# Kernel tuning notes

Hardware: AMD Instinct MI355X
Metric: run time of the kernel (lower is better)

The kernel has to match this reference:

```python
import jax, jax.numpy as jnp
import numpy as np

T, B, D_IN, D_LAT = 512, 64, 512, 1024


def setup_inputs() -> dict:
    key = jax.random.key(0)
    ks = jax.random.split(key, 9)
    s_in = 1.0 / np.sqrt(D_IN + D_LAT)
    inp = {
        "x": jax.random.normal(ks[0], (T, B, D_IN), dtype=jnp.float32),
        "Wf": jax.random.normal(ks[1], (D_LAT, D_IN + D_LAT), dtype=jnp.float32) * s_in,
        "bf": jax.random.normal(ks[2], (D_LAT,), dtype=jnp.float32) * s_in,
        "Wi": jax.random.normal(ks[3], (D_LAT, D_IN + D_LAT), dtype=jnp.float32) * s_in,
        "bi": jax.random.normal(ks[4], (D_LAT,), dtype=jnp.float32) * s_in,
        "Wc": jax.random.normal(ks[5], (D_LAT, D_IN + D_LAT), dtype=jnp.float32) * s_in,
        "bc": jax.random.normal(ks[6], (D_LAT,), dtype=jnp.float32) * s_in,
        "Wo": jax.random.normal(ks[7], (D_LAT, D_IN + D_LAT), dtype=jnp.float32) * s_in,
        "bo": jax.random.normal(ks[8], (D_LAT,), dtype=jnp.float32) * s_in,
    }
    return inp


def reference(x, Wf, bf, Wi, bi, Wc, bc, Wo, bo):
    # x: [T, B, D_in]. Same math as 4 separate gate linears on concat(x, h),
    # expressed as one fused gate GEMM per step (concat weights along out dim).
    length, batch, _ = x.shape
    latent = Wf.shape[0]
    W = jnp.concatenate([Wf, Wi, Wc, Wo], axis=0)            # [4L, D_in+L]
    b = jnp.concatenate([bf, bi, bc, bo], axis=0)            # [4L]
    Wx, Wh = W[:, : x.shape[-1]], W[:, x.shape[-1]:]         # split concat input
    # Precompute input contribution for all timesteps: [T, B, 4L]
    xg = jnp.einsum('tbd,gd->tbg', x, Wx) + b

    def step(carry, xg_t):
        h, c = carry
        g = xg_t + h @ Wh.T                                   # [B, 4L]
        f = jax.nn.sigmoid(g[:, 0 * latent:1 * latent])
        i = jax.nn.sigmoid(g[:, 1 * latent:2 * latent])
        cand = jnp.tanh(g[:, 2 * latent:3 * latent])
        o = jax.nn.sigmoid(g[:, 3 * latent:4 * latent])
        c_new = f * c + i * cand
        h_new = o * jnp.tanh(c_new)
        return (h_new, c_new), h_new

    h0 = jnp.zeros((batch, latent), dtype=x.dtype)
    c0 = jnp.zeros((batch, latent), dtype=x.dtype)  # self.ct zeros init
    _, hs = jax.lax.scan(step, (h0, c0), xg)
    return hs  # [T, B, latent]
```

## Files before the change

kernel.cpp:

```cpp
#include <hip/hip_runtime.h>
#include <hip/hip_bf16.h>


typedef __attribute__((ext_vector_type(8))) short short8;
typedef __attribute__((ext_vector_type(4))) short short4v;
typedef __attribute__((ext_vector_type(4))) float f32x4;

#define T_STEPS 512
#define BATCH   64
#define DIN     512
#define DLAT    1024
#define NWG     128
#define LPW     8

#define WS_H    4096
#define WS_XG   (4096 + 262144)

#define MFMA(a, b, c) __builtin_amdgcn_mfma_f32_16x16x32_bf16((a), (b), (c), 0, 0, 0)

static __device__ __forceinline__ unsigned short f2bf(float f) {
  unsigned u = __builtin_bit_cast(unsigned, f);
  u = (u + 0x7FFFu + ((u >> 16) & 1u)) >> 16;
  return (unsigned short)u;
}
static __device__ __forceinline__ float bf2f(unsigned short s) {
  unsigned u = ((unsigned)s) << 16;
  return __builtin_bit_cast(float, u);
}
static __device__ __forceinline__ float sigf(float x) {
  return 1.0f / (1.0f + __expf(-x));
}
static __device__ __forceinline__ float tanhfast(float x) {
  return 2.0f / (1.0f + __expf(-2.0f * x)) - 1.0f;
}
static __device__ __forceinline__ short8 packbf(f32x4 a, f32x4 b) {
  short8 s;
  s[0]=(short)f2bf(a[0]); s[1]=(short)f2bf(a[1]); s[2]=(short)f2bf(a[2]); s[3]=(short)f2bf(a[3]);
  s[4]=(short)f2bf(b[0]); s[5]=(short)f2bf(b[1]); s[6]=(short)f2bf(b[2]); s[7]=(short)f2bf(b[3]);
  return s;
}

__global__ __launch_bounds__(256, 2) void lstm_phase1(
    const float* __restrict__ x,
    const float* __restrict__ Wf, const float* __restrict__ bfp,
    const float* __restrict__ Wi, const float* __restrict__ bip,
    const float* __restrict__ Wc, const float* __restrict__ bcp,
    const float* __restrict__ Wo, const float* __restrict__ bop,
    unsigned short* __restrict__ xg)
{
  __shared__ __align__(16) short lds[BATCH * DIN];
  const int tid  = threadIdx.x;
  const int nb   = blockIdx.x;
  const int tb4  = blockIdx.y;
  const int lane = tid & 63;
  const int wv   = tid >> 6;
  const int cc   = lane & 15;
  const int q    = lane >> 4;

  const int wg = nb * 4 + wv;
  const int jj = wg * LPW + (cc & 7);
  short8 bw[2][16];
  #pragma unroll
  for (int T = 0; T < 2; ++T) {
    const float* Wp = (T == 0) ? (cc < 8 ? Wf : Wi) : (cc < 8 ? Wc : Wo);
    const float* base = Wp + (size_t)jj * (DIN + DLAT);
    #pragma unroll
    for (int k = 0; k < 16; ++k) {
      const f32x4* p = (const f32x4*)(base + k * 32 + q * 8);
      bw[T][k] = packbf(p[0], p[1]);
    }
  }
  float biasv[2];
  biasv[0] = (cc < 8 ? bfp : bip)[jj];
  biasv[1] = (cc < 8 ? bcp : bop)[jj];

  for (int tt = 0; tt < 4; ++tt) {
    const int tb = tb4 * 4 + tt;

    const float* xs = x + (size_t)tb * (BATCH * DIN);
    #pragma unroll
    for (int it = 0; it < 16; ++it) {
      int c = tid + 256 * it;
      int row = c >> 6, kc = c & 63;
      const f32x4* p = (const f32x4*)(xs + row * DIN + kc * 8);
      f32x4 v0 = p[0], v1 = p[1];
      int byte = (row * (DIN * 2) + kc * 16) ^ ((row & 7) << 4);
      *(short8*)((char*)lds + byte) = packbf(v0, v1);
    }
    __syncthreads();

    f32x4 acc[4][2] = {};
    #pragma unroll
    for (int k = 0; k < 16; ++k) {
      #pragma unroll
      for (int m = 0; m < 4; ++m) {
        int row = m * 16 + cc;
        int byte = (row * (DIN * 2) + (k * 32 + q * 8) * 2) ^ ((row & 7) << 4);
        short8 a = *(const short8*)((const char*)lds + byte);
        acc[m][0] = MFMA(a, bw[0][k], acc[m][0]);
        acc[m][1] = MFMA(a, bw[1][k], acc[m][1]);
      }
    }
    __syncthreads();

    #pragma unroll
    for (int T = 0; T < 2; ++T) {
      float bias = biasv[T];
      #pragma unroll
      for (int m = 0; m < 4; ++m) {
        f32x4 g = acc[m][T];
        short4v s;
        s[0] = (short)f2bf(g[0] + bias);
        s[1] = (short)f2bf(g[1] + bias);
        s[2] = (short)f2bf(g[2] + bias);
        s[3] = (short)f2bf(g[3] + bias);
        size_t idx = ((((size_t)tb * NWG + wg) * 4 + m) * 2 + T) * 64 + lane;
        *(short4v*)(xg + idx * 4) = s;
      }
    }
  }
}

__global__ __launch_bounds__(256, 1) void lstm_phase2(
    const float* __restrict__ Wf, const float* __restrict__ Wi,
    const float* __restrict__ Wc, const float* __restrict__ Wo,
    const unsigned short* __restrict__ xg,
    unsigned short* __restrict__ hbuf,
    unsigned int* __restrict__ flags,
    float* __restrict__ out)
{
  const int tid  = threadIdx.x;
  const int lane = tid & 63;
  const int wv   = tid >> 6;
  const int wg   = blockIdx.x;
  const int cc   = lane & 15;
  const int q    = lane >> 4;
  const int jj   = wg * LPW + (cc & 7);

  __shared__ unsigned short lds_h[4][16][8];
  __shared__ float          lds_o[4][16][8];

  short8 wh[2][32];
  #pragma unroll
  for (int T = 0; T < 2; ++T) {
    const float* Wp = (T == 0) ? (cc < 8 ? Wf : Wi) : (cc < 8 ? Wc : Wo);
    const float* base = Wp + (size_t)jj * (DIN + DLAT) + DIN;
    #pragma unroll
    for (int k = 0; k < 32; ++k) {
      const f32x4* p = (const f32x4*)(base + k * 32 + q * 8);
      wh[T][k] = packbf(p[0], p[1]);
    }
  }

  f32x4 cst = {0.f, 0.f, 0.f, 0.f};
  const unsigned short* xbase = xg + (((size_t)wg * 4 + wv) * 2) * 256 + (size_t)lane * 4;
  const int arow = wv * 16 + cc;

  short4v xp0 = *(const short4v*)(xbase);
  short4v xp1 = *(const short4v*)(xbase + 256);

  for (int t = 0; t < T_STEPS; ++t) {
    if (t > 0) {
      if (wv == 0) {
        const unsigned int* fp = flags + lane;
        for (;;) {
          unsigned a1 = __hip_atomic_load(fp,      __ATOMIC_RELAXED, __HIP_MEMORY_SCOPE_AGENT);
          unsigned a2 = __hip_atomic_load(fp + 64, __ATOMIC_RELAXED, __HIP_MEMORY_SCOPE_AGENT);
          if (__all(a1 >= (unsigned)t && a2 >= (unsigned)t)) break;
          __builtin_amdgcn_s_sleep(1);
        }
      }
      __syncthreads();
    }

    f32x4 acc0 = {0.f,0.f,0.f,0.f}, acc1 = {0.f,0.f,0.f,0.f};
    if (t > 0) {
      const unsigned long long* hq = (const unsigned long long*)
          (hbuf + (((t & 1) ^ 1) << 16) + arow * DLAT);
      short8 a[16];
      #pragma unroll
      for (int k = 0; k < 16; ++k) {
        unsigned long long lo = __hip_atomic_load(hq + q*2 + k*8,     __ATOMIC_RELAXED, __HIP_MEMORY_SCOPE_AGENT);
        unsigned long long hi = __hip_atomic_load(hq + q*2 + k*8 + 1, __ATOMIC_RELAXED, __HIP_MEMORY_SCOPE_AGENT);
        union { unsigned long long u[2]; short8 s; } cv; cv.u[0]=lo; cv.u[1]=hi;
        a[k] = cv.s;
      }
      #pragma unroll
      for (int k = 0; k < 16; ++k) {
        acc0 = MFMA(a[k], wh[0][k], acc0);
        acc1 = MFMA(a[k], wh[1][k], acc1);
      }
      #pragma unroll
      for (int k = 0; k < 16; ++k) {
        unsigned long long lo = __hip_atomic_load(hq + q*2 + (16+k)*8,     __ATOMIC_RELAXED, __HIP_MEMORY_SCOPE_AGENT);
        unsigned long long hi = __hip_atomic_load(hq + q*2 + (16+k)*8 + 1, __ATOMIC_RELAXED, __HIP_MEMORY_SCOPE_AGENT);
        union { unsigned long long u[2]; short8 s; } cv; cv.u[0]=lo; cv.u[1]=hi;
        a[k] = cv.s;
      }
      #pragma unroll
      for (int k = 0; k < 16; ++k) {
        acc0 = MFMA(a[k], wh[0][16 + k], acc0);
        acc1 = MFMA(a[k], wh[1][16 + k], acc1);
      }
    }

    f32x4 g0, g1;
    #pragma unroll
    for (int r = 0; r < 4; ++r) {
      g0[r] = acc0[r] + bf2f((unsigned short)xp0[r]);
      g1[r] = acc1[r] + bf2f((unsigned short)xp1[r]);
    }

    f32x4 g0x, g1x;
    #pragma unroll
    for (int r = 0; r < 4; ++r) {
      g0x[r] = __shfl_xor(g0[r], 8, 64);
      g1x[r] = __shfl_xor(g1[r], 8, 64);
    }
    const bool lo = (cc < 8);
    float hv[4];
    #pragma unroll
    for (int r = 0; r < 4; ++r) {
      float fpre = lo ? g0[r]  : g0x[r];
      float ipre = lo ? g0x[r] : g0[r];
      float cpre = lo ? g1[r]  : g1x[r];
      float opre = lo ? g1x[r] : g1[r];
      float fg = sigf(fpre), ig = sigf(ipre), cd = tanhfast(cpre), og = sigf(opre);
      float cn = fg * cst[r] + ig * cd;
      cst[r] = cn;
      hv[r] = og * tanhfast(cn);
    }

    if (lo) {
      #pragma unroll
      for (int r = 0; r < 4; ++r) {
        lds_h[wv][q * 4 + r][cc] = f2bf(hv[r]);
        lds_o[wv][q * 4 + r][cc] = hv[r];
      }
    }
    __syncthreads();

    {
      unsigned short* hw = hbuf + ((t & 1) << 16);
      float* op = out + (size_t)t * (BATCH * DLAT);
      if (lane < 32) {
        int row = lane >> 1, half = lane & 1;
        unsigned long long v = *(const unsigned long long*)&lds_h[wv][row][half * 4];
        int b = wv * 16 + row;
        __hip_atomic_store((unsigned long long*)(hw + b * DLAT + wg * LPW + half * 4), v,
                           __ATOMIC_RELAXED, __HIP_MEMORY_SCOPE_AGENT);
      }
      {
        int row = lane >> 2, quarter = lane & 3;
        unsigned long long v = *(const unsigned long long*)&lds_o[wv][row][quarter * 2];
        int b = wv * 16 + row;
        *(unsigned long long*)(op + b * DLAT + wg * LPW + quarter * 2) = v;
      }
    }

    asm volatile("s_waitcnt vmcnt(0)" ::: "memory");
    __syncthreads();
    if (tid == 0)
      __hip_atomic_store(flags + wg, (unsigned)(t + 1), __ATOMIC_RELAXED, __HIP_MEMORY_SCOPE_AGENT);

    {
      int tn = (t + 1 < T_STEPS) ? t + 1 : t;
      const unsigned short* xn = xbase + ((size_t)tn << 18);
      xp0 = *(const short4v*)(xn);
      xp1 = *(const short4v*)(xn + 256);
    }
  }
}

extern "C" void kernel_launch(void* const* d_in, const int* in_sizes, int n_in,
                              void* d_out, int out_size, void* d_ws, size_t ws_size,
                              hipStream_t stream) {
  (void)in_sizes; (void)n_in; (void)out_size; (void)ws_size;
  const float* x   = (const float*)d_in[0];
  const float* Wf  = (const float*)d_in[1];
  const float* bfp = (const float*)d_in[2];
  const float* Wi  = (const float*)d_in[3];
  const float* bip = (const float*)d_in[4];
  const float* Wc  = (const float*)d_in[5];
  const float* bcp = (const float*)d_in[6];
  const float* Wo  = (const float*)d_in[7];
  const float* bop = (const float*)d_in[8];
  float* out = (float*)d_out;

  unsigned int*   flags = (unsigned int*)d_ws;
  unsigned short* hbuf  = (unsigned short*)((char*)d_ws + WS_H);
  unsigned short* xg    = (unsigned short*)((char*)d_ws + WS_XG);

  hipMemsetAsync(d_ws, 0, 4096, stream);
  lstm_phase1<<<dim3(32, 128), 256, 0, stream>>>(x, Wf, bfp, Wi, bip, Wc, bcp, Wo, bop, xg);
  lstm_phase2<<<dim3(NWG), 256, 0, stream>>>(Wf, Wi, Wc, Wo, xg, hbuf, flags, out);
}
```

Before: 6.313 ms.

## Shrink recurrent grid to 32 workgroups with LDS-staged swizzled h broadcast

The recurrent phase now runs on 32 workgroups instead of 128. Each wave owns 8 latent units across all 64 batch rows, giving 4 M-tiles per wave. The full h vector is bulk-copied from global into a swizzled LDS staging buffer in two halves, and MFMA A-operands are read from LDS. Each wave no longer issues its own per-lane global atomic loads. The aim is to cut the grid-barrier fan-in (fewer flags to poll) and redundant global h reads. The cost is 4x more MFMA work per workgroup on the serial critical path, plus extra syncthreads.

```diff
diff --git a/kernel.cpp b/kernel.cpp
--- a/kernel.cpp
+++ b/kernel.cpp
@@ -5,18 +5,20 @@
 typedef __attribute__((ext_vector_type(8))) short short8;
 typedef __attribute__((ext_vector_type(4))) short short4v;
 typedef __attribute__((ext_vector_type(4))) float f32x4;
+typedef unsigned long long ull;
 
 #define T_STEPS 512
 #define BATCH   64
 #define DIN     512
 #define DLAT    1024
-#define NWG     128
-#define LPW     8
+#define NWG2    32
 
 #define WS_H    4096
 #define WS_XG   (4096 + 262144)
 
 #define MFMA(a, b, c) __builtin_amdgcn_mfma_f32_16x16x32_bf16((a), (b), (c), 0, 0, 0)
+#define AT_LD(p)    __hip_atomic_load((p), __ATOMIC_RELAXED, __HIP_MEMORY_SCOPE_AGENT)
+#define AT_ST(p, v) __hip_atomic_store((p), (v), __ATOMIC_RELAXED, __HIP_MEMORY_SCOPE_AGENT)
 
 static __device__ __forceinline__ unsigned short f2bf(float f) {
   unsigned u = __builtin_bit_cast(unsigned, f);
@@ -58,7 +60,7 @@
   const int q    = lane >> 4;
 
   const int wg = nb * 4 + wv;
-  const int jj = wg * LPW + (cc & 7);
+  const int jj = wg * 8 + (cc & 7);
   short8 bw[2][16];
   #pragma unroll
   for (int T = 0; T < 2; ++T) {
@@ -76,7 +78,6 @@
 
   for (int tt = 0; tt < 4; ++tt) {
     const int tb = tb4 * 4 + tt;
-
     const float* xs = x + (size_t)tb * (BATCH * DIN);
     #pragma unroll
     for (int it = 0; it < 16; ++it) {
@@ -114,8 +115,8 @@
         s[1] = (short)f2bf(g[1] + bias);
         s[2] = (short)f2bf(g[2] + bias);
         s[3] = (short)f2bf(g[3] + bias);
-        size_t idx = ((((size_t)tb * NWG + wg) * 4 + m) * 2 + T) * 64 + lane;
-        *(short4v*)(xg + idx * 4) = s;
+        size_t idx = (size_t)tb * 1024 + (size_t)wg * 8 + m * 2 + T;
+        *(short4v*)(xg + idx * 256 + lane * 4) = s;
       }
     }
   }
@@ -129,16 +130,18 @@
     unsigned int* __restrict__ flags,
     float* __restrict__ out)
 {
+  __shared__ __align__(16) ull stage[8192];
+  unsigned short* lds_h = (unsigned short*)stage;
+  float*          lds_o = (float*)((char*)stage + 4096);
+
   const int tid  = threadIdx.x;
   const int lane = tid & 63;
   const int wv   = tid >> 6;
   const int wg   = blockIdx.x;
   const int cc   = lane & 15;
   const int q    = lane >> 4;
-  const int jj   = wg * LPW + (cc & 7);
-
-  __shared__ unsigned short lds_h[4][16][8];
-  __shared__ float          lds_o[4][16][8];
+  const int swz  = (cc & 7) << 4;
+  const int jj   = wg * 32 + wv * 8 + (cc & 7);
 
   short8 wh[2][32];
   #pragma unroll
@@ -152,123 +155,138 @@
     }
   }
 
-  f32x4 cst = {0.f, 0.f, 0.f, 0.f};
-  const unsigned short* xbase = xg + (((size_t)wg * 4 + wv) * 2) * 256 + (size_t)lane * 4;
-  const int arow = wv * 16 + cc;
-
-  short4v xp0 = *(const short4v*)(xbase);
-  short4v xp1 = *(const short4v*)(xbase + 256);
+  f32x4 cst[4] = {};
+  const unsigned short* xbase = xg + (size_t)(wg * 32 + wv * 8) * 256 + lane * 4;
+  short4v xp0[4], xp1[4];
+  #pragma unroll
+  for (int m = 0; m < 4; ++m) {
+    xp0[m] = *(const short4v*)(xbase + (m * 2 + 0) * 256);
+    xp1[m] = *(const short4v*)(xbase + (m * 2 + 1) * 256);
+  }
+
+  const ull* hb = (const ull*)hbuf;
 
   for (int t = 0; t < T_STEPS; ++t) {
+    f32x4 acc[4][2] = {};
+
     if (t > 0) {
-      if (wv == 0) {
-        const unsigned int* fp = flags + lane;
+      {
+        const unsigned int* fp = flags + (lane & 31);
         for (;;) {
-          unsigned a1 = __hip_atomic_load(fp,      __ATOMIC_RELAXED, __HIP_MEMORY_SCOPE_AGENT);
-          unsigned a2 = __hip_atomic_load(fp + 64, __ATOMIC_RELAXED, __HIP_MEMORY_SCOPE_AGENT);
-          if (__all(a1 >= (unsigned)t && a2 >= (unsigned)t)) break;
+          unsigned a = AT_LD(fp);
+          if (__all(a >= (unsigned)t)) break;
           __builtin_amdgcn_s_sleep(1);
         }
       }
+      const ull* hsrc = hb + (size_t)((t & 1) ^ 1) * 16384;
+      const char* sb = (const char*)stage;
+      ull areg[32];
+
+      #pragma unroll
+      for (int i = 0; i < 32; ++i) areg[i] = AT_LD(hsrc + i * 256 + tid);
+      #pragma unroll
+      for (int i = 0; i < 32; ++i) stage[i * 256 + tid] = areg[i];
       __syncthreads();
-    }
-
-    f32x4 acc0 = {0.f,0.f,0.f,0.f}, acc1 = {0.f,0.f,0.f,0.f};
-    if (t > 0) {
-      const unsigned long long* hq = (const unsigned long long*)
-          (hbuf + (((t & 1) ^ 1) << 16) + arow * DLAT);
-      short8 a[16];
-      #pragma unroll
-      for (int k = 0; k < 16; ++k) {
-        unsigned long long lo = __hip_atomic_load(hq + q*2 + k*8,     __ATOMIC_RELAXED, __HIP_MEMORY_SCOPE_AGENT);
-        unsigned long long hi = __hip_atomic_load(hq + q*2 + k*8 + 1, __ATOMIC_RELAXED, __HIP_MEMORY_SCOPE_AGENT);
-        union { unsigned long long u[2]; short8 s; } cv; cv.u[0]=lo; cv.u[1]=hi;
-        a[k] = cv.s;
-      }
-      #pragma unroll
-      for (int k = 0; k < 16; ++k) {
-        acc0 = MFMA(a[k], wh[0][k], acc0);
-        acc1 = MFMA(a[k], wh[1][k], acc1);
-      }
-      #pragma unroll
-      for (int k = 0; k < 16; ++k) {
-        unsigned long long lo = __hip_atomic_load(hq + q*2 + (16+k)*8,     __ATOMIC_RELAXED, __HIP_MEMORY_SCOPE_AGENT);
-        unsigned long long hi = __hip_atomic_load(hq + q*2 + (16+k)*8 + 1, __ATOMIC_RELAXED, __HIP_MEMORY_SCOPE_AGENT);
-        union { unsigned long long u[2]; short8 s; } cv; cv.u[0]=lo; cv.u[1]=hi;
-        a[k] = cv.s;
-      }
-      #pragma unroll
-      for (int k = 0; k < 16; ++k) {
-        acc0 = MFMA(a[k], wh[0][16 + k], acc0);
-        acc1 = MFMA(a[k], wh[1][16 + k], acc1);
-      }
-    }
-
-    f32x4 g0, g1;
-    #pragma unroll
-    for (int r = 0; r < 4; ++r) {
-      g0[r] = acc0[r] + bf2f((unsigned short)xp0[r]);
-      g1[r] = acc1[r] + bf2f((unsigned short)xp1[r]);
-    }
-
-    f32x4 g0x, g1x;
-    #pragma unroll
-    for (int r = 0; r < 4; ++r) {
-      g0x[r] = __shfl_xor(g0[r], 8, 64);
-      g1x[r] = __shfl_xor(g1[r], 8, 64);
-    }
+
+      #pragma unroll
+      for (int i = 0; i < 32; ++i) areg[i] = AT_LD(hsrc + 8192 + i * 256 + tid);
+      #pragma unroll
+      for (int m = 0; m < 2; ++m) {
+        const int rb = (m * 16 + cc) * 2048;
+        #pragma unroll
+        for (int k = 0; k < 32; ++k) {
+          short8 a = *(const short8*)(sb + ((rb + k * 64 + q * 16) ^ swz));
+          acc[m][0] = MFMA(a, wh[0][k], acc[m][0]);
+          acc[m][1] = MFMA(a, wh[1][k], acc[m][1]);
+        }
+      }
+      __syncthreads();
+
+      #pragma unroll
+      for (int i = 0; i < 32; ++i) stage[i * 256 + tid] = areg[i];
+      __syncthreads();
+      #pragma unroll
+      for (int m = 2; m < 4; ++m) {
+        const int rb = ((m - 2) * 16 + cc) * 2048;
+        #pragma unroll
+        for (int k = 0; k < 32; ++k) {
+          short8 a = *(const short8*)(sb + ((rb + k * 64 + q * 16) ^ swz));
+          acc[m][0] = MFMA(a, wh[0][k], acc[m][0]);
+          acc[m][1] = MFMA(a, wh[1][k], acc[m][1]);
+        }
+      }
+      __syncthreads();
+    }
+
     const bool lo = (cc < 8);
-    float hv[4];
-    #pragma unroll
-    for (int r = 0; r < 4; ++r) {
-      float fpre = lo ? g0[r]  : g0x[r];
-      float ipre = lo ? g0x[r] : g0[r];
-      float cpre = lo ? g1[r]  : g1x[r];
-      float opre = lo ? g1x[r] : g1[r];
-      float fg = sigf(fpre), ig = sigf(ipre), cd = tanhfast(cpre), og = sigf(opre);
-      float cn = fg * cst[r] + ig * cd;
-      cst[r] = cn;
-      hv[r] = og * tanhfast(cn);
-    }
-
-    if (lo) {
+    #pragma unroll
+    for (int m = 0; m < 4; ++m) {
+      f32x4 g0, g1;
       #pragma unroll
       for (int r = 0; r < 4; ++r) {
-        lds_h[wv][q * 4 + r][cc] = f2bf(hv[r]);
-        lds_o[wv][q * 4 + r][cc] = hv[r];
+        g0[r] = acc[m][0][r] + bf2f((unsigned short)xp0[m][r]);
+        g1[r] = acc[m][1][r] + bf2f((unsigned short)xp1[m][r]);
+      }
+      f32x4 g0x, g1x;
+      #pragma unroll
+      for (int r = 0; r < 4; ++r) {
+        g0x[r] = __shfl_xor(g0[r], 8, 64);
+        g1x[r] = __shfl_xor(g1[r], 8, 64);
+      }
+      float hv[4];
+      #pragma unroll
+      for (int r = 0; r < 4; ++r) {
+        float fpre = lo ? g0[r]  : g0x[r];
+        float ipre = lo ? g0x[r] : g0[r];
+        float cpre = lo ? g1[r]  : g1x[r];
+        float opre = lo ? g1x[r] : g1[r];
+        float fg = sigf(fpre), ig = sigf(ipre), cd = tanhfast(cpre), og = sigf(opre);
+        float cn = fg * cst[m][r] + ig * cd;
+        cst[m][r] = cn;
+        hv[r] = og * tanhfast(cn);
+      }
+      if (lo) {
+        #pragma unroll
+        for (int r = 0; r < 4; ++r) {
+          int b = m * 16 + q * 4 + r;
+          lds_h[b * 32 + wv * 8 + cc] = f2bf(hv[r]);
+          lds_o[b * 32 + wv * 8 + cc] = hv[r];
+        }
       }
     }
     __syncthreads();
 
     {
-      unsigned short* hw = hbuf + ((t & 1) << 16);
-      float* op = out + (size_t)t * (BATCH * DLAT);
-      if (lane < 32) {
-        int row = lane >> 1, half = lane & 1;
-        unsigned long long v = *(const unsigned long long*)&lds_h[wv][row][half * 4];
-        int b = wv * 16 + row;
-        __hip_atomic_store((unsigned long long*)(hw + b * DLAT + wg * LPW + half * 4), v,
-                           __ATOMIC_RELAXED, __HIP_MEMORY_SCOPE_AGENT);
-      }
-      {
-        int row = lane >> 2, quarter = lane & 3;
-        unsigned long long v = *(const unsigned long long*)&lds_o[wv][row][quarter * 2];
-        int b = wv * 16 + row;
-        *(unsigned long long*)(op + b * DLAT + wg * LPW + quarter * 2) = v;
-      }
-    }
-
+      const int row = tid >> 2, i = tid & 3;
+      ull v0 = ((const ull*)lds_h)[row * 8 + i * 2 + 0];
+      ull v1 = ((const ull*)lds_h)[row * 8 + i * 2 + 1];
+      char* hw = (char*)hbuf + (size_t)(t & 1) * 131072;
+      int base = row * 2048 + wg * 64 + i * 16;
+      AT_ST((ull*)(hw + ((base + 0) ^ ((row & 7) << 4))), v0);
+      AT_ST((ull*)(hw + ((base + 8) ^ ((row & 7) << 4))), v1);
+    }
     asm volatile("s_waitcnt vmcnt(0)" ::: "memory");
     __syncthreads();
-    if (tid == 0)
-      __hip_atomic_store(flags + wg, (unsigned)(t + 1), __ATOMIC_RELAXED, __HIP_MEMORY_SCOPE_AGENT);
-
+    if (tid == 0) AT_ST(flags + wg, (unsigned)(t + 1));
+
+    {
+      const int row = tid >> 2, i = tid & 3;
+      const f32x4* src = (const f32x4*)(lds_o + row * 32 + i * 8);
+      f32x4 o0 = src[0], o1 = src[1];
+      float* op = out + (size_t)t * (BATCH * DLAT) + row * DLAT + wg * 32 + i * 8;
+      *(f32x4*)op = o0;
+      *(f32x4*)(op + 4) = o1;
+    }
     {
       int tn = (t + 1 < T_STEPS) ? t + 1 : t;
       const unsigned short* xn = xbase + ((size_t)tn << 18);
-      xp0 = *(const short4v*)(xn);
-      xp1 = *(const short4v*)(xn + 256);
-    }
+      #pragma unroll
+      for (int m = 0; m < 4; ++m) {
+        xp0[m] = *(const short4v*)(xn + (m * 2 + 0) * 256);
+        xp1[m] = *(const short4v*)(xn + (m * 2 + 1) * 256);
+      }
+    }
+    __syncthreads();
   }
 }
 
@@ -293,5 +311,5 @@
 
   hipMemsetAsync(d_ws, 0, 4096, stream);
   lstm_phase1<<<dim3(32, 128), 256, 0, stream>>>(x, Wf, bfp, Wi, bip, Wc, bcp, Wo, bop, xg);
-  lstm_phase2<<<dim3(NWG), 256, 0, stream>>>(Wf, Wi, Wc, Wo, xg, hbuf, flags, out);
-}
+  lstm_phase2<<<dim3(NWG2), 256, 0, stream>>>(Wf, Wi, Wc, Wo, xg, hbuf, flags, out);
+}
```

After: 9.007 ms. 42.7% more time.

## Read recurrent h from fp32 output instead of separate bf16 h buffer

Applied to the files above, without the earlier changes.

Removes the separate double-buffered bf16 hidden-state buffer. Each step now reads h(t-1) directly from the fp32 output tensor and converts it to bf16 in registers with v_cvt_pk_bf16_f32. All four waves poll the flags themselves, which replaces the wave-0 poll followed by a barrier, and the output store becomes an agent-scope atomic store. This cuts one global write stream and one LDS staging array per step, but each step must read twice as many bytes of h, uses plain (non-atomic) loads for cross-block data, and adds a barrier at the end of each step.

```diff
diff --git a/kernel.cpp b/kernel.cpp
--- a/kernel.cpp
+++ b/kernel.cpp
@@ -5,18 +5,19 @@
 typedef __attribute__((ext_vector_type(8))) short short8;
 typedef __attribute__((ext_vector_type(4))) short short4v;
 typedef __attribute__((ext_vector_type(4))) float f32x4;
+typedef unsigned long long ull;
 
 #define T_STEPS 512
 #define BATCH   64
 #define DIN     512
 #define DLAT    1024
 #define NWG     128
-#define LPW     8
-
-#define WS_H    4096
-#define WS_XG   (4096 + 262144)
+
+#define WS_XG   4096
 
 #define MFMA(a, b, c) __builtin_amdgcn_mfma_f32_16x16x32_bf16((a), (b), (c), 0, 0, 0)
+#define AT_LD(p)    __hip_atomic_load((p), __ATOMIC_RELAXED, __HIP_MEMORY_SCOPE_AGENT)
+#define AT_ST(p, v) __hip_atomic_store((p), (v), __ATOMIC_RELAXED, __HIP_MEMORY_SCOPE_AGENT)
 
 static __device__ __forceinline__ unsigned short f2bf(float f) {
   unsigned u = __builtin_bit_cast(unsigned, f);
@@ -38,6 +39,14 @@
   s[0]=(short)f2bf(a[0]); s[1]=(short)f2bf(a[1]); s[2]=(short)f2bf(a[2]); s[3]=(short)f2bf(a[3]);
   s[4]=(short)f2bf(b[0]); s[5]=(short)f2bf(b[1]); s[6]=(short)f2bf(b[2]); s[7]=(short)f2bf(b[3]);
   return s;
+}
+static __device__ __forceinline__ short8 cvt8(f32x4 a, f32x4 b) {
+  union { unsigned u[4]; short8 s; } r;
+  asm("v_cvt_pk_bf16_f32 %0, %1, %2" : "=v"(r.u[0]) : "v"(a[0]), "v"(a[1]));
+  asm("v_cvt_pk_bf16_f32 %0, %1, %2" : "=v"(r.u[1]) : "v"(a[2]), "v"(a[3]));
+  asm("v_cvt_pk_bf16_f32 %0, %1, %2" : "=v"(r.u[2]) : "v"(b[0]), "v"(b[1]));
+  asm("v_cvt_pk_bf16_f32 %0, %1, %2" : "=v"(r.u[3]) : "v"(b[2]), "v"(b[3]));
+  return r.s;
 }
 
 __global__ __launch_bounds__(256, 2) void lstm_phase1(
@@ -58,7 +67,7 @@
   const int q    = lane >> 4;
 
   const int wg = nb * 4 + wv;
-  const int jj = wg * LPW + (cc & 7);
+  const int jj = wg * 8 + (cc & 7);
   short8 bw[2][16];
   #pragma unroll
   for (int T = 0; T < 2; ++T) {
@@ -76,7 +85,6 @@
 
   for (int tt = 0; tt < 4; ++tt) {
     const int tb = tb4 * 4 + tt;
-
     const float* xs = x + (size_t)tb * (BATCH * DIN);
     #pragma unroll
     for (int it = 0; it < 16; ++it) {
@@ -125,20 +133,18 @@
     const float* __restrict__ Wf, const float* __restrict__ Wi,
     const float* __restrict__ Wc, const float* __restrict__ Wo,
     const unsigned short* __restrict__ xg,
-    unsigned short* __restrict__ hbuf,
     unsigned int* __restrict__ flags,
     float* __restrict__ out)
 {
+  __shared__ float lds_o[4][16][8];
+
   const int tid  = threadIdx.x;
   const int lane = tid & 63;
   const int wv   = tid >> 6;
   const int wg   = blockIdx.x;
   const int cc   = lane & 15;
   const int q    = lane >> 4;
-  const int jj   = wg * LPW + (cc & 7);
-
-  __shared__ unsigned short lds_h[4][16][8];
-  __shared__ float          lds_o[4][16][8];
+  const int jj   = wg * 8 + (cc & 7);
 
   short8 wh[2][32];
   #pragma unroll
@@ -160,47 +166,34 @@
   short4v xp1 = *(const short4v*)(xbase + 256);
 
   for (int t = 0; t < T_STEPS; ++t) {
+    f32x4 acc0 = {0.f,0.f,0.f,0.f}, acc1 = {0.f,0.f,0.f,0.f};
+
     if (t > 0) {
-      if (wv == 0) {
+      {
         const unsigned int* fp = flags + lane;
         for (;;) {
-          unsigned a1 = __hip_atomic_load(fp,      __ATOMIC_RELAXED, __HIP_MEMORY_SCOPE_AGENT);
-          unsigned a2 = __hip_atomic_load(fp + 64, __ATOMIC_RELAXED, __HIP_MEMORY_SCOPE_AGENT);
+          unsigned a1 = AT_LD(fp);
+          unsigned a2 = AT_LD(fp + 64);
           if (__all(a1 >= (unsigned)t && a2 >= (unsigned)t)) break;
           __builtin_amdgcn_s_sleep(1);
         }
       }
-      __syncthreads();
-    }
-
-    f32x4 acc0 = {0.f,0.f,0.f,0.f}, acc1 = {0.f,0.f,0.f,0.f};
-    if (t > 0) {
-      const unsigned long long* hq = (const unsigned long long*)
-          (hbuf + (((t & 1) ^ 1) << 16) + arow * DLAT);
-      short8 a[16];
-      #pragma unroll
-      for (int k = 0; k < 16; ++k) {
-        unsigned long long lo = __hip_atomic_load(hq + q*2 + k*8,     __ATOMIC_RELAXED, __HIP_MEMORY_SCOPE_AGENT);
-        unsigned long long hi = __hip_atomic_load(hq + q*2 + k*8 + 1, __ATOMIC_RELAXED, __HIP_MEMORY_SCOPE_AGENT);
-        union { unsigned long long u[2]; short8 s; } cv; cv.u[0]=lo; cv.u[1]=hi;
-        a[k] = cv.s;
-      }
-      #pragma unroll
-      for (int k = 0; k < 16; ++k) {
-        acc0 = MFMA(a[k], wh[0][k], acc0);
-        acc1 = MFMA(a[k], wh[1][k], acc1);
-      }
-      #pragma unroll
-      for (int k = 0; k < 16; ++k) {
-        unsigned long long lo = __hip_atomic_load(hq + q*2 + (16+k)*8,     __ATOMIC_RELAXED, __HIP_MEMORY_SCOPE_AGENT);
-        unsigned long long hi = __hip_atomic_load(hq + q*2 + (16+k)*8 + 1, __ATOMIC_RELAXED, __HIP_MEMORY_SCOPE_AGENT);
-        union { unsigned long long u[2]; short8 s; } cv; cv.u[0]=lo; cv.u[1]=hi;
-        a[k] = cv.s;
-      }
-      #pragma unroll
-      for (int k = 0; k < 16; ++k) {
-        acc0 = MFMA(a[k], wh[0][16 + k], acc0);
-        acc1 = MFMA(a[k], wh[1][16 + k], acc1);
+      const float* hrow = out + (((size_t)(t - 1)) << 16) + arow * DLAT + q * 8;
+      #pragma unroll
+      for (int chunk = 0; chunk < 2; ++chunk) {
+        f32x4 r0[16], r1[16];
+        #pragma unroll
+        for (int k = 0; k < 16; ++k) {
+          const f32x4* p = (const f32x4*)(hrow + (chunk * 16 + k) * 32);
+          r0[k] = p[0];
+          r1[k] = p[1];
+        }
+        #pragma unroll
+        for (int k = 0; k < 16; ++k) {
+          short8 a = cvt8(r0[k], r1[k]);
+          acc0 = MFMA(a, wh[0][chunk * 16 + k], acc0);
+          acc1 = MFMA(a, wh[1][chunk * 16 + k], acc1);
+        }
       }
     }
 
@@ -210,7 +203,6 @@
       g0[r] = acc0[r] + bf2f((unsigned short)xp0[r]);
       g1[r] = acc1[r] + bf2f((unsigned short)xp1[r]);
     }
-
     f32x4 g0x, g1x;
     #pragma unroll
     for (int r = 0; r < 4; ++r) {
@@ -233,35 +225,18 @@
 
     if (lo) {
       #pragma unroll
-      for (int r = 0; r < 4; ++r) {
-        lds_h[wv][q * 4 + r][cc] = f2bf(hv[r]);
-        lds_o[wv][q * 4 + r][cc] = hv[r];
-      }
-    }
-    __syncthreads();
-
+      for (int r = 0; r < 4; ++r) lds_o[wv][q * 4 + r][cc] = hv[r];
+    }
+    __syncthreads();
     {
-      unsigned short* hw = hbuf + ((t & 1) << 16);
-      float* op = out + (size_t)t * (BATCH * DLAT);
-      if (lane < 32) {
-        int row = lane >> 1, half = lane & 1;
-        unsigned long long v = *(const unsigned long long*)&lds_h[wv][row][half * 4];
-        int b = wv * 16 + row;
-        __hip_atomic_store((unsigned long long*)(hw + b * DLAT + wg * LPW + half * 4), v,
-                           __ATOMIC_RELAXED, __HIP_MEMORY_SCOPE_AGENT);
-      }
-      {
-        int row = lane >> 2, quarter = lane & 3;
-        unsigned long long v = *(const unsigned long long*)&lds_o[wv][row][quarter * 2];
-        int b = wv * 16 + row;
-        *(unsigned long long*)(op + b * DLAT + wg * LPW + quarter * 2) = v;
-      }
-    }
-
+      const int row = tid >> 2, i = tid & 3;
+      ull v = ((const ull*)lds_o)[row * 4 + i];
+      float* op = out + ((size_t)t << 16) + row * DLAT + wg * 8;
+      AT_ST((ull*)op + i, v);
+    }
     asm volatile("s_waitcnt vmcnt(0)" ::: "memory");
     __syncthreads();
-    if (tid == 0)
-      __hip_atomic_store(flags + wg, (unsigned)(t + 1), __ATOMIC_RELAXED, __HIP_MEMORY_SCOPE_AGENT);
+    if (tid == 0) AT_ST(flags + wg, (unsigned)(t + 1));
 
     {
       int tn = (t + 1 < T_STEPS) ? t + 1 : t;
@@ -269,6 +244,7 @@
       xp0 = *(const short4v*)(xn);
       xp1 = *(const short4v*)(xn + 256);
     }
+    __syncthreads();
   }
 }
 
@@ -288,10 +264,9 @@
   float* out = (float*)d_out;
 
   unsigned int*   flags = (unsigned int*)d_ws;
-  unsigned short* hbuf  = (unsigned short*)((char*)d_ws + WS_H);
   unsigned short* xg    = (unsigned short*)((char*)d_ws + WS_XG);
 
   hipMemsetAsync(d_ws, 0, 4096, stream);
   lstm_phase1<<<dim3(32, 128), 256, 0, stream>>>(x, Wf, bfp, Wi, bip, Wc, bcp, Wo, bop, xg);
-  lstm_phase2<<<dim3(NWG), 256, 0, stream>>>(Wf, Wi, Wc, Wo, xg, hbuf, flags, out);
-}
+  lstm_phase2<<<dim3(NWG), 256, 0, stream>>>(Wf, Wi, Wc, Wo, xg, flags, out);
+}
```

After: 8.421 ms. 33.4% more time.
